# Kernel tuning notes

Hardware: AMD Instinct MI355X
Metric: run time of the kernel (lower is better)

The kernel has to match this reference:

```python
import jax, jax.numpy as jnp
import numpy as np

B, T_SEQ, STATE, DIM_IN, DIM_K, DIM_V, LAYER = 8, 2048, 128, 1024, 64, 64, 4
T = T_SEQ + 2 * STATE  # 2304
LAMBDA_INIT = 0.8 - 0.6 * float(np.exp(-0.3 * LAYER))
NEG = -1e30


def setup_inputs() -> dict:
    key = jax.random.key(0)
    ks = jax.random.split(key, 20)
    def w(k, shape):
        return jax.random.normal(k, shape, dtype=jnp.float32) * 0.02
    inp = {"x": jax.random.normal(ks[0], (B, T, DIM_IN), dtype=jnp.float32)}
    # projection weights stored as (in, out) so y = x @ W
    inp["Wq"] = w(ks[1], (DIM_IN, 2 * DIM_K)); inp["Wk"] = w(ks[2], (DIM_IN, 2 * DIM_K)); inp["Wv"] = w(ks[3], (DIM_IN, 2 * DIM_V))
    inp["Wq_ss"] = w(ks[4], (DIM_IN, 2 * DIM_K)); inp["Wk_ss"] = w(ks[5], (DIM_IN, 2 * DIM_K)); inp["Wv_ss"] = w(ks[6], (DIM_IN, 2 * DIM_V))
    inp["Wq_se"] = w(ks[7], (DIM_IN, 2 * DIM_K)); inp["Wk_se"] = w(ks[8], (DIM_IN, 2 * DIM_K)); inp["Wv_se"] = w(ks[9], (DIM_IN, 2 * DIM_V))
    # layernorm params (torch defaults: ones/zeros)
    inp["g_in"] = jnp.ones((DIM_IN,), jnp.float32); inp["b_in"] = jnp.zeros((DIM_IN,), jnp.float32)
    inp["g_ss"] = jnp.ones((DIM_IN,), jnp.float32); inp["b_ss"] = jnp.zeros((DIM_IN,), jnp.float32)
    inp["g_se"] = jnp.ones((DIM_IN,), jnp.float32); inp["b_se"] = jnp.zeros((DIM_IN,), jnp.float32)
    inp["g_out"] = jnp.ones((2 * DIM_V,), jnp.float32); inp["b_out"] = jnp.zeros((2 * DIM_V,), jnp.float32)
    # lambda gate params
    inp["lq1"] = jax.random.normal(ks[10], (1, DIM_K), jnp.float32)
    inp["lq2"] = jax.random.normal(ks[11], (1, DIM_K), jnp.float32)
    inp["lk1"] = jax.random.normal(ks[12], (DIM_K, 1), jnp.float32)
    inp["lk2"] = jax.random.normal(ks[13], (DIM_K, 1), jnp.float32)
    return inp


def _ln(z, g, b, eps=1e-5):
    m = jnp.mean(z, axis=-1, keepdims=True)
    v = jnp.mean((z - m) ** 2, axis=-1, keepdims=True)
    return (z - m) * jax.lax.rsqrt(v + eps) * g + b


def reference(x, Wq, Wk, Wv, Wq_ss, Wk_ss, Wv_ss, Wq_se, Wk_se, Wv_se,
              g_in, b_in, g_ss, b_ss, g_se, b_se, g_out, b_out,
              lq1, lq2, lk1, lk2):
    # extract_state: split off state tokens at both ends
    xs, xm, xe = x[:, :STATE], x[:, STATE:-STATE], x[:, -STATE:]
    xm = _ln(xm, g_in, b_in)
    xs = _ln(xs, g_ss, b_ss)
    xe = _ln(xe, g_se, b_se)
    q = jnp.concatenate([xs @ Wq_ss, xm @ Wq, xe @ Wq_se], axis=1)  # (B,T,2K)
    k = jnp.concatenate([xs @ Wk_ss, xm @ Wk, xe @ Wk_se], axis=1)
    v = jnp.concatenate([xs @ Wv_ss, xm @ Wv, xe @ Wv_se], axis=1)  # (B,T,2V)
    q1, q2 = q[..., :DIM_K], q[..., DIM_K:]
    k1, k2 = k[..., :DIM_K], k[..., DIM_K:]
    scale = 1.0 / np.sqrt(DIM_K)
    t = q.shape[1]
    causal = jnp.triu(jnp.full((t, t), NEG, dtype=q.dtype), k=1)  # (T,T)
    s1 = jnp.einsum('btd,bsd->bts', q1, k1) * scale + causal
    s2 = jnp.einsum('btd,bsd->bts', q2, k2) * scale + causal
    a1 = jax.nn.softmax(s1, axis=-1)
    a2 = jax.nn.softmax(s2, axis=-1)
    o1 = jnp.einsum('bts,bsd->btd', a1, v)
    o2 = jnp.einsum('bts,bsd->btd', a2, v)
    lam = (jnp.exp(lq1 @ lk1) - jnp.exp(lq2 @ lk2))[0, 0] + LAMBDA_INIT
    att = o1 - lam * o2
    return _ln(att, g_out, b_out)
```

## Files before the change

### kernel.cpp

```cpp
#include <hip/hip_runtime.h>
#include <hip/hip_bf16.h>
#include <stdint.h>

#define B_ 8
#define T_ 2304
#define DIN 1024
#define LAMBDA_INIT_F 0.6192834728526788f

typedef __bf16 bf16x8 __attribute__((ext_vector_type(8)));
typedef float f32x4 __attribute__((ext_vector_type(4)));

__device__ __forceinline__ unsigned short f2bf(float f) {
    union { float f; unsigned int u; } v; v.f = f;
    unsigned int u = v.u;
    unsigned int r = (u + 0x7FFFu + ((u >> 16) & 1u)) >> 16;
    return (unsigned short)r;
}

__device__ __forceinline__ unsigned int pack2bf(float lo, float hi) {
    return ((unsigned int)f2bf(hi) << 16) | (unsigned int)f2bf(lo);
}

__device__ __forceinline__ float bf2f(unsigned short u) {
    union { unsigned int u; float f; } v; v.u = ((unsigned int)u) << 16;
    return v.f;
}

__global__ __launch_bounds__(256) void k_wtrans(
    const float* w0, const float* w1, const float* w2,
    const float* w3, const float* w4, const float* w5,
    const float* w6, const float* w7, const float* w8,
    unsigned short* __restrict__ wt)
{
    __shared__ float tile[64][65];
    int bx = blockIdx.x;
    int mat = bx >> 5;
    int tl = bx & 31;
    int tx = tl & 15;
    int ty = tl >> 4;
    const float* srcs[9] = {w0, w1, w2, w3, w4, w5, w6, w7, w8};
    const float* src = srcs[mat];
    int k0 = tx * 64, c0 = ty * 64;
    int t = threadIdx.x;
    int r = t >> 2, cg = (t & 3) << 4;
    const float* p = src + (size_t)(k0 + r) * 128 + c0 + cg;
#pragma unroll
    for (int i = 0; i < 4; ++i) {
        float4 v = *(const float4*)(p + i * 4);
        tile[r][cg + i * 4 + 0] = v.x;
        tile[r][cg + i * 4 + 1] = v.y;
        tile[r][cg + i * 4 + 2] = v.z;
        tile[r][cg + i * 4 + 3] = v.w;
    }
    __syncthreads();
    int seg = mat / 3, m = mat % 3;
    int crow = seg * 384 + m * 128 + c0 + r;
    unsigned short* dst = wt + (size_t)crow * 1024 + k0 + cg;
    __align__(16) unsigned short ob[16];
#pragma unroll
    for (int i = 0; i < 16; ++i) ob[i] = f2bf(tile[cg + i][r]);
    *(uint4*)(dst) = *(const uint4*)(ob);
    *(uint4*)(dst + 8) = *(const uint4*)(ob + 8);
}

__global__ __launch_bounds__(256) void k_ln(
    const float* __restrict__ x,
    const float* __restrict__ g_in, const float* __restrict__ b_in,
    const float* __restrict__ g_ss, const float* __restrict__ b_ss,
    const float* __restrict__ g_se, const float* __restrict__ b_se,
    unsigned short* __restrict__ xbf)
{
    int row = (blockIdx.x << 2) + (threadIdx.x >> 6);
    int l = threadIdx.x & 63;
    int t = row % T_;
    const float* gv; const float* bv;
    if (t < 128)       { gv = g_ss; bv = b_ss; }
    else if (t < 2176) { gv = g_in; bv = b_in; }
    else               { gv = g_se; bv = b_se; }
    const float* xp = x + (size_t)row * DIN + l * 4;
    float4 v0 = *(const float4*)(xp);
    float4 v1 = *(const float4*)(xp + 256);
    float4 v2 = *(const float4*)(xp + 512);
    float4 v3 = *(const float4*)(xp + 768);
    float s  = v0.x + v0.y + v0.z + v0.w + v1.x + v1.y + v1.z + v1.w
             + v2.x + v2.y + v2.z + v2.w + v3.x + v3.y + v3.z + v3.w;
    float s2 = v0.x*v0.x + v0.y*v0.y + v0.z*v0.z + v0.w*v0.w
             + v1.x*v1.x + v1.y*v1.y + v1.z*v1.z + v1.w*v1.w
             + v2.x*v2.x + v2.y*v2.y + v2.z*v2.z + v2.w*v2.w
             + v3.x*v3.x + v3.y*v3.y + v3.z*v3.z + v3.w*v3.w;
#pragma unroll
    for (int off = 1; off <= 32; off <<= 1) {
        s  += __shfl_xor(s,  off);
        s2 += __shfl_xor(s2, off);
    }
    float mean = s * (1.f / 1024.f);
    float rstd = rsqrtf(s2 * (1.f / 1024.f) - mean * mean + 1e-5f);
    unsigned short* op = xbf + (size_t)row * DIN + l * 4;
    const float* gp = gv + l * 4;
    const float* bp = bv + l * 4;
#pragma unroll
    for (int k = 0; k < 4; ++k) {
        float4 vv = (k == 0) ? v0 : (k == 1) ? v1 : (k == 2) ? v2 : v3;
        float4 gk = *(const float4*)(gp + k * 256);
        float4 bk = *(const float4*)(bp + k * 256);
        uint2 o;
        o.x = pack2bf((vv.x - mean) * rstd * gk.x + bk.x,
                      (vv.y - mean) * rstd * gk.y + bk.y);
        o.y = pack2bf((vv.z - mean) * rstd * gk.z + bk.z,
                      (vv.w - mean) * rstd * gk.w + bk.w);
        *(uint2*)(op + k * 256) = o;
    }
}

__global__ __launch_bounds__(512, 4) void k_proj2(
    const unsigned short* __restrict__ xbf,
    const unsigned short* __restrict__ wt,
    unsigned short* __restrict__ qo,
    unsigned short* __restrict__ ko,
    unsigned short* __restrict__ vto)
{
    __shared__ __align__(16) char smem[81920];

    int bid = blockIdx.x;
    int mt = bid >> 1, ch = bid & 1;
    int bb = mt / 18, tt = mt % 18;
    int seg = (tt == 0) ? 0 : ((tt < 17) ? 1 : 2);
    size_t arow0 = (size_t)mt * 128;
    int ncol0 = ch * 192;
    int wrow0 = seg * 384 + ncol0;

    int tid = threadIdx.x;
    int w = tid >> 6, l = tid & 63;
    int wr = w >> 2, wc = w & 3;
    int g4 = l >> 4, cr = l & 15;

    int rA0 = tid >> 3, cS = (tid & 7) << 4;
    const char* srcA0 = (const char*)xbf + (arow0 + rA0) * 2048 + cS;
    const char* srcA1 = srcA0 + (size_t)64 * 2048;
    int dA0 = rA0 * 128 + (cS ^ ((rA0 & 7) << 4));
    int dA1 = dA0 + 64 * 128;
    const char* srcW0 = (const char*)wt + (size_t)(wrow0 + rA0) * 2048 + cS;
    const char* srcW1 = srcW0 + (size_t)64 * 2048;
    const char* srcW2 = srcW0 + (size_t)128 * 2048;
    int dW0 = dA0, dW1 = dA0 + 64 * 128, dW2 = dA0 + 128 * 128;

    {
        uint4 a0 = *(const uint4*)srcA0;
        uint4 a1 = *(const uint4*)srcA1;
        uint4 w0 = *(const uint4*)srcW0;
        uint4 w1 = *(const uint4*)srcW1;
        uint4 w2 = *(const uint4*)srcW2;
        *(uint4*)(smem + dA0) = a0;
        *(uint4*)(smem + dA1) = a1;
        *(uint4*)(smem + 32768 + dW0) = w0;
        *(uint4*)(smem + 32768 + dW1) = w1;
        *(uint4*)(smem + 32768 + dW2) = w2;
    }
    __syncthreads();

    f32x4 acc[4][3] = {};
    for (int ks = 0; ks < 16; ++ks) {
        bool pf = (ks < 15);
        uint4 pa0, pa1, pw0, pw1, pw2;
        if (pf) {
            size_t o = (size_t)(ks + 1) * 128;
            pa0 = *(const uint4*)(srcA0 + o);
            pa1 = *(const uint4*)(srcA1 + o);
            pw0 = *(const uint4*)(srcW0 + o);
            pw1 = *(const uint4*)(srcW1 + o);
            pw2 = *(const uint4*)(srcW2 + o);
        }
        const char* Ab = smem + (ks & 1) * 16384;
        const char* Wb = smem + 32768 + (ks & 1) * 24576;
        __builtin_amdgcn_s_setprio(1);
#pragma unroll
        for (int kk = 0; kk < 2; ++kk) {
            int kb = kk * 64 + g4 * 16;
            bf16x8 af[4];
#pragma unroll
            for (int r4 = 0; r4 < 4; ++r4) {
                int rr = wr * 64 + r4 * 16 + cr;
                af[r4] = *(const bf16x8*)(Ab + rr * 128 + (kb ^ ((rr & 7) << 4)));
            }
            bf16x8 bfr[3];
#pragma unroll
            for (int nt = 0; nt < 3; ++nt) {
                int c = wc * 48 + nt * 16 + cr;
                bfr[nt] = *(const bf16x8*)(Wb + c * 128 + (kb ^ ((c & 7) << 4)));
            }
#pragma unroll
            for (int r4 = 0; r4 < 4; ++r4)
#pragma unroll
                for (int nt = 0; nt < 3; ++nt)
                    acc[r4][nt] = __builtin_amdgcn_mfma_f32_16x16x32_bf16(af[r4], bfr[nt], acc[r4][nt], 0, 0, 0);
        }
        __builtin_amdgcn_s_setprio(0);
        __syncthreads();
        if (pf) {
            char* An = smem + ((ks + 1) & 1) * 16384;
            char* Wn = smem + 32768 + ((ks + 1) & 1) * 24576;
            *(uint4*)(An + dA0) = pa0;
            *(uint4*)(An + dA1) = pa1;
            *(uint4*)(Wn + dW0) = pw0;
            *(uint4*)(Wn + dW1) = pw1;
            *(uint4*)(Wn + dW2) = pw2;
        }
        __syncthreads();
    }

#pragma unroll
    for (int r4 = 0; r4 < 4; ++r4) {
        size_t grow = arow0 + wr * 64 + r4 * 16 + g4 * 4;
#pragma unroll
        for (int nt = 0; nt < 3; ++nt) {
            int c = ncol0 + wc * 48 + nt * 16 + cr;
            f32x4 a = acc[r4][nt];
            if (c < 128) {
#pragma unroll
                for (int g = 0; g < 4; ++g)
                    qo[(grow + g) * 128 + c] = f2bf(a[g]);
            } else if (c < 256) {
#pragma unroll
                for (int g = 0; g < 4; ++g)
                    ko[(grow + g) * 128 + (c - 128)] = f2bf(a[g]);
            } else {
                int cv = c - 256;
                int trow = tt * 128 + wr * 64 + r4 * 16 + g4 * 4;
                uint2 o;
                o.x = pack2bf(a[0], a[1]);
                o.y = pack2bf(a[2], a[3]);
                *(uint2*)(vto + ((size_t)bb * 128 + cv) * T_ + trow) = o;
            }
        }
    }
}

__global__ __launch_bounds__(512, 2) void k_attn(
    const unsigned short* __restrict__ qp_,
    const unsigned short* __restrict__ kp_,
    const unsigned short* __restrict__ vp_,
    const float* __restrict__ lq1, const float* __restrict__ lq2,
    const float* __restrict__ lk1, const float* __restrict__ lk2,
    const float* __restrict__ g_out, const float* __restrict__ b_out,
    unsigned short* __restrict__ opart,
    float* __restrict__ mlpart,
    float* __restrict__ out)
{
    __shared__ __align__(16) char smem[69632];

    int bid = blockIdx.x;
    int b = bid & 7;
    int u = 71 - (bid >> 3);
    int j, ci;
    if (u < 12)      { j = u; ci = 0; }
    else if (u < 36) { int v = u - 12; j = 12 + (v >> 1); ci = v & 1; }
    else             { int v = u - 36; j = 24 + v / 3; ci = v % 3; }
    int nch = (j + 12) / 12;
    int c0 = ci * 12;
    int ntile = min(12, j + 1 - c0);
    int t0 = j * 64;

    int tid = threadIdx.x;
    int w8 = tid >> 6;
    int qg = w8 & 3;
    int p  = w8 >> 2;
    int l = tid & 63;
    int g4 = l >> 4, q = l & 15;
    int q_g = t0 + qg * 16 + q;
    int grp = tid >> 8;
    int uu = tid & 255;

    int rK = uu >> 2, cK = (uu & 3) << 6;
    const char* srcK0 = (const char*)(kp_ + ((size_t)b * T_ + rK) * 128) + cK;
    int rV = uu >> 1, cV = (uu & 1) << 6;
    const char* srcV0 = (const char*)(vp_ + ((size_t)b * 128 + rV) * T_) + cV;
    int swK = (rK & 7) << 4;
    char* KwB = smem + grp * 16384 + rK * 256;
    int oko0 = (cK +  0) ^ swK, oko1 = (cK + 16) ^ swK;
    int oko2 = (cK + 32) ^ swK, oko3 = (cK + 48) ^ swK;
    int swV = (rV & 7) << 4;
    char* VwB = smem + 32768 + grp * 16384 + rV * 128;
    int ovo0 = (cV +  0) ^ swV, ovo1 = (cV + 16) ^ swV;
    int ovo2 = (cV + 32) ^ swV, ovo3 = (cV + 48) ^ swV;

    bf16x8 qf[2][2];
#pragma unroll
    for (int br = 0; br < 2; ++br)
#pragma unroll
        for (int h = 0; h < 2; ++h)
            qf[br][h] = *(const bf16x8*)(qp_ + ((size_t)b * T_ + q_g) * 128 + br * 64 + h * 32 + g4 * 8);

    if (grp < ntile) {
        const char* sK = srcK0 + (size_t)(c0 + grp) * 16384;
        uint4 ka0 = *(const uint4*)(sK);
        uint4 ka1 = *(const uint4*)(sK + 16);
        uint4 ka2 = *(const uint4*)(sK + 32);
        uint4 ka3 = *(const uint4*)(sK + 48);
        const char* sV = srcV0 + (size_t)(c0 + grp) * 128;
        uint4 va0 = *(const uint4*)(sV);
        uint4 va1 = *(const uint4*)(sV + 16);
        uint4 va2 = *(const uint4*)(sV + 32);
        uint4 va3 = *(const uint4*)(sV + 48);
        *(uint4*)(KwB + oko0) = ka0;
        *(uint4*)(KwB + oko1) = ka1;
        *(uint4*)(KwB + oko2) = ka2;
        *(uint4*)(KwB + oko3) = ka3;
        *(uint4*)(VwB + ovo0) = va0;
        *(uint4*)(VwB + ovo1) = va1;
        *(uint4*)(VwB + ovo2) = va2;
        *(uint4*)(VwB + ovo3) = va3;
    }
    __syncthreads();

    float mrun[2] = {-1e30f, -1e30f};
    float lrun[2] = {0.f, 0.f};
    f32x4 oacc[2][8] = {};
    const char* Kb = smem + p * 16384;
    const char* Vb = smem + 32768 + p * 16384;

    int nph = (ntile + 1) >> 1;
    for (int t = 0; t < nph; ++t) {
        int lpf = 2 * (t + 1) + grp;
        bool pfv = (lpf < ntile);
        uint4 ka0, ka1, ka2, ka3, va0, va1, va2, va3;
        if (pfv) {
            const char* sK = srcK0 + (size_t)(c0 + lpf) * 16384;
            ka0 = *(const uint4*)(sK);
            ka1 = *(const uint4*)(sK + 16);
            ka2 = *(const uint4*)(sK + 32);
            ka3 = *(const uint4*)(sK + 48);
            const char* sV = srcV0 + (size_t)(c0 + lpf) * 128;
            va0 = *(const uint4*)(sV);
            va1 = *(const uint4*)(sV + 16);
            va2 = *(const uint4*)(sV + 32);
            va3 = *(const uint4*)(sV + 48);
        }

        int lt = 2 * t + p;
        if (lt < ntile) {
            int kt = c0 + lt;
            bool diag = (kt == j);
            unsigned int pk[2][4][2];
#pragma unroll
            for (int br = 0; br < 2; ++br) {
                f32x4 s[4] = {};
                __builtin_amdgcn_s_setprio(1);
#pragma unroll
                for (int h = 0; h < 2; ++h) {
#pragma unroll
                    for (int t4 = 0; t4 < 4; ++t4) {
                        int rk = t4 * 16 + q;
                        bf16x8 kf = *(const bf16x8*)(Kb + rk * 256 + ((br * 128 + h * 64 + g4 * 16) ^ ((rk & 7) << 4)));
                        s[t4] = __builtin_amdgcn_mfma_f32_16x16x32_bf16(kf, qf[br][h], s[t4], 0, 0, 0);
                    }
                }
                __builtin_amdgcn_s_setprio(0);
                float sv[16];
                float mx = -1e30f;
#pragma unroll
                for (int t4 = 0; t4 < 4; ++t4)
#pragma unroll
                    for (int r = 0; r < 4; ++r) {
                        float v = s[t4][r] * 0.125f;
                        if (diag) {
                            int kv_g = kt * 64 + t4 * 16 + g4 * 4 + r;
                            if (kv_g > q_g) v = -1e30f;
                        }
                        sv[t4 * 4 + r] = v;
                        mx = fmaxf(mx, v);
                    }
                mx = fmaxf(mx, __shfl_xor(mx, 16));
                mx = fmaxf(mx, __shfl_xor(mx, 32));
                float mn;
                if (__all(mx <= mrun[br] + 8.f)) {
                    mn = mrun[br];
                } else {
                    mn = fmaxf(mrun[br], mx);
                    float sf = __expf(mrun[br] - mn);
                    mrun[br] = mn;
                    lrun[br] *= sf;
#pragma unroll
                    for (int dblk = 0; dblk < 8; ++dblk)
#pragma unroll
                        for (int r = 0; r < 4; ++r)
                            oacc[br][dblk][r] *= sf;
                }
                float pr[16];
                float rs = 0.f;
#pragma unroll
                for (int i = 0; i < 16; ++i) {
                    pr[i] = __expf(sv[i] - mn);
                    rs += pr[i];
                }
                rs += __shfl_xor(rs, 16);
                rs += __shfl_xor(rs, 32);
                lrun[br] += rs;
#pragma unroll
                for (int t4 = 0; t4 < 4; ++t4) {
                    pk[br][t4][0] = pack2bf(pr[t4 * 4 + 0], pr[t4 * 4 + 1]);
                    pk[br][t4][1] = pack2bf(pr[t4 * 4 + 2], pr[t4 * 4 + 3]);
                }
            }
#pragma unroll
            for (int h = 0; h < 2; ++h) {
                bf16x8 pb[2];
                int s0 = q + (((g4 * 2) & 3) << 4);
                int s1 = q + (((g4 * 2 + 1) & 3) << 4);
                int sel = g4 >> 1;
#pragma unroll
                for (int br = 0; br < 2; ++br) {
                    unsigned int m0a = (unsigned int)__shfl((int)pk[br][2 * h][0], s0);
                    unsigned int m0b = (unsigned int)__shfl((int)pk[br][2 * h + 1][0], s0);
                    unsigned int m1a = (unsigned int)__shfl((int)pk[br][2 * h][1], s0);
                    unsigned int m1b = (unsigned int)__shfl((int)pk[br][2 * h + 1][1], s0);
                    unsigned int m2a = (unsigned int)__shfl((int)pk[br][2 * h][0], s1);
                    unsigned int m2b = (unsigned int)__shfl((int)pk[br][2 * h + 1][0], s1);
                    unsigned int m3a = (unsigned int)__shfl((int)pk[br][2 * h][1], s1);
                    unsigned int m3b = (unsigned int)__shfl((int)pk[br][2 * h + 1][1], s1);
                    union { unsigned int uv[4]; bf16x8 v; } pu;
                    pu.uv[0] = sel ? m0b : m0a;
                    pu.uv[1] = sel ? m1b : m1a;
                    pu.uv[2] = sel ? m2b : m2a;
                    pu.uv[3] = sel ? m3b : m3a;
                    pb[br] = pu.v;
                }
                __builtin_amdgcn_s_setprio(1);
#pragma unroll
                for (int dblk = 0; dblk < 8; ++dblk) {
                    int rv = dblk * 16 + q;
                    bf16x8 vf = *(const bf16x8*)(Vb + rv * 128 + ((h * 64 + g4 * 16) ^ ((rv & 7) << 4)));
                    oacc[0][dblk] = __builtin_amdgcn_mfma_f32_16x16x32_bf16(vf, pb[0], oacc[0][dblk], 0, 0, 0);
                    oacc[1][dblk] = __builtin_amdgcn_mfma_f32_16x16x32_bf16(vf, pb[1], oacc[1][dblk], 0, 0, 0);
                }
                __builtin_amdgcn_s_setprio(0);
            }
        }
        __syncthreads();
        if (pfv) {
            *(uint4*)(KwB + oko0) = ka0;
            *(uint4*)(KwB + oko1) = ka1;
            *(uint4*)(KwB + oko2) = ka2;
            *(uint4*)(KwB + oko3) = ka3;
            *(uint4*)(VwB + ovo0) = va0;
            *(uint4*)(VwB + ovo1) = va1;
            *(uint4*)(VwB + ovo2) = va2;
            *(uint4*)(VwB + ovo3) = va3;
        }
        __syncthreads();
    }

    float* Osh = (float*)smem;
    float* Msh = (float*)(smem + 65536);
    if (p == 1) {
        int base = qg * 4096 + l;
#pragma unroll
        for (int br = 0; br < 2; ++br)
#pragma unroll
            for (int dblk = 0; dblk < 8; ++dblk)
#pragma unroll
                for (int r = 0; r < 4; ++r)
                    Osh[base + (br * 32 + dblk * 4 + r) * 64] = oacc[br][dblk][r];
        float4 ml;
        ml.x = mrun[0]; ml.y = lrun[0]; ml.z = mrun[1]; ml.w = lrun[1];
        *(float4*)(Msh + (qg * 64 + l) * 4) = ml;
    }
    __syncthreads();
    if (p == 0) {
        float4 ml = *(const float4*)(Msh + (qg * 64 + l) * 4);
        float m1v[2] = {ml.x, ml.z}, l1v[2] = {ml.y, ml.w};
        float lfin[2], mst[2];
#pragma unroll
        for (int br = 0; br < 2; ++br) {
            float mstar = fmaxf(mrun[br], m1v[br]);
            float a0 = __expf(mrun[br] - mstar);
            float a1 = __expf(m1v[br] - mstar);
            lfin[br] = a0 * lrun[br] + a1 * l1v[br];
            mst[br] = mstar;
            int base = qg * 4096 + l;
#pragma unroll
            for (int dblk = 0; dblk < 8; ++dblk)
#pragma unroll
                for (int r = 0; r < 4; ++r)
                    oacc[br][dblk][r] = a0 * oacc[br][dblk][r]
                        + a1 * Osh[base + (br * 32 + dblk * 4 + r) * 64];
        }

        int row = qg * 16 + q;
        if (nch == 1) {
            float pa = lq1[l] * lk1[l];
            float pb2 = lq2[l] * lk2[l];
#pragma unroll
            for (int off = 32; off >= 1; off >>= 1) {
                pa += __shfl_xor(pa, off);
                pb2 += __shfl_xor(pb2, off);
            }
            float lam = __expf(pa) - __expf(pb2) + LAMBDA_INIT_F;

            float att[8][4];
            float sm = 0.f;
            float inv1 = 1.f / lfin[0], inv2 = 1.f / lfin[1];
#pragma unroll
            for (int dblk = 0; dblk < 8; ++dblk)
#pragma unroll
                for (int r = 0; r < 4; ++r) {
                    float a = oacc[0][dblk][r] * inv1 - lam * (oacc[1][dblk][r] * inv2);
                    att[dblk][r] = a;
                    sm += a;
                }
            sm += __shfl_xor(sm, 16);
            sm += __shfl_xor(sm, 32);
            float mean = sm * (1.f / 128.f);
            float sv2 = 0.f;
#pragma unroll
            for (int dblk = 0; dblk < 8; ++dblk)
#pragma unroll
                for (int r = 0; r < 4; ++r) {
                    float d = att[dblk][r] - mean;
                    sv2 += d * d;
                }
            sv2 += __shfl_xor(sv2, 16);
            sv2 += __shfl_xor(sv2, 32);
            float rstd = rsqrtf(sv2 * (1.f / 128.f) + 1e-5f);

            float* orow = out + ((size_t)b * T_ + q_g) * 128;
#pragma unroll
            for (int dblk = 0; dblk < 8; ++dblk) {
                int d0 = dblk * 16 + g4 * 4;
                float4 o;
                o.x = (att[dblk][0] - mean) * rstd * g_out[d0 + 0] + b_out[d0 + 0];
                o.y = (att[dblk][1] - mean) * rstd * g_out[d0 + 1] + b_out[d0 + 1];
                o.z = (att[dblk][2] - mean) * rstd * g_out[d0 + 2] + b_out[d0 + 2];
                o.w = (att[dblk][3] - mean) * rstd * g_out[d0 + 3] + b_out[d0 + 3];
                *(float4*)(orow + d0) = o;
            }
        } else {
            int slot = (b * 36 + j) * 3 + ci;
            char* ob = (char*)opart + (size_t)slot * 32768;
#pragma unroll
            for (int br = 0; br < 2; ++br) {
#pragma unroll
                for (int dblk = 0; dblk < 8; ++dblk) {
                    uint2 o;
                    o.x = pack2bf(oacc[br][dblk][0], oacc[br][dblk][1]);
                    o.y = pack2bf(oacc[br][dblk][2], oacc[br][dblk][3]);
                    *(uint2*)(ob + br * 16384 + row * 256 + (dblk * 16 + g4 * 4) * 2) = o;
                }
                float2 mlv;
                mlv.x = mst[br];
                mlv.y = lfin[br];
                *(float2*)(mlpart + ((size_t)slot * 128 + br * 64 + row) * 2) = mlv;
            }
        }
    }
}

__global__ __launch_bounds__(512) void k_merge(
    const unsigned short* __restrict__ opart,
    const float* __restrict__ mlpart,
    const float* __restrict__ lq1, const float* __restrict__ lq2,
    const float* __restrict__ lk1, const float* __restrict__ lk2,
    const float* __restrict__ g_out, const float* __restrict__ b_out,
    float* __restrict__ out)
{
    int bid = blockIdx.x;
    int b = bid & 7;
    int j = 12 + (bid >> 3);
    int nch = (j + 12) / 12;
    int tid = threadIdx.x;
    int row = tid >> 3;
    int d0 = (tid & 7) * 16;
    int l = tid & 63;

    float pa = lq1[l] * lk1[l];
    float pb = lq2[l] * lk2[l];
#pragma unroll
    for (int off = 32; off >= 1; off >>= 1) {
        pa += __shfl_xor(pa, off);
        pb += __shfl_xor(pb, off);
    }
    float lam = __expf(pa) - __expf(pb) + LAMBDA_INIT_F;

    int slotb = (b * 36 + j) * 3;
    float res[2][16];
#pragma unroll
    for (int br = 0; br < 2; ++br) {
        float m0 = mlpart[((size_t)(slotb + 0) * 128 + br * 64 + row) * 2];
        float l0 = mlpart[((size_t)(slotb + 0) * 128 + br * 64 + row) * 2 + 1];
        float m1 = mlpart[((size_t)(slotb + 1) * 128 + br * 64 + row) * 2];
        float l1 = mlpart[((size_t)(slotb + 1) * 128 + br * 64 + row) * 2 + 1];
        float m2 = -1e30f, l2 = 0.f;
        if (nch == 3) {
            m2 = mlpart[((size_t)(slotb + 2) * 128 + br * 64 + row) * 2];
            l2 = mlpart[((size_t)(slotb + 2) * 128 + br * 64 + row) * 2 + 1];
        }
        float mstar = fmaxf(fmaxf(m0, m1), m2);
        float w0 = __expf(m0 - mstar);
        float w1 = __expf(m1 - mstar);
        float w2 = (nch == 3) ? __expf(m2 - mstar) : 0.f;
        float lsum = w0 * l0 + w1 * l1 + w2 * l2;

        float acc[16] = {};
#pragma unroll
        for (int c = 0; c < 3; ++c) {
            if (c >= nch) break;
            float wc = (c == 0) ? w0 : (c == 1) ? w1 : w2;
            const char* ob = (const char*)opart + (size_t)(slotb + c) * 32768
                           + br * 16384 + row * 256 + d0 * 2;
            uint4 v0 = *(const uint4*)(ob);
            uint4 v1 = *(const uint4*)(ob + 16);
            const unsigned int vv[8] = {v0.x, v0.y, v0.z, v0.w, v1.x, v1.y, v1.z, v1.w};
#pragma unroll
            for (int i = 0; i < 8; ++i) {
                acc[i * 2]     += wc * bf2f((unsigned short)(vv[i] & 0xFFFF));
                acc[i * 2 + 1] += wc * bf2f((unsigned short)(vv[i] >> 16));
            }
        }
        float inv = 1.f / lsum;
#pragma unroll
        for (int i = 0; i < 16; ++i) res[br][i] = acc[i] * inv;
    }

    float att[16];
    float sm = 0.f;
#pragma unroll
    for (int i = 0; i < 16; ++i) {
        att[i] = res[0][i] - lam * res[1][i];
        sm += att[i];
    }
    sm += __shfl_xor(sm, 1);
    sm += __shfl_xor(sm, 2);
    sm += __shfl_xor(sm, 4);
    float mean = sm * (1.f / 128.f);
    float sv2 = 0.f;
#pragma unroll
    for (int i = 0; i < 16; ++i) {
        float d = att[i] - mean;
        sv2 += d * d;
    }
    sv2 += __shfl_xor(sv2, 1);
    sv2 += __shfl_xor(sv2, 2);
    sv2 += __shfl_xor(sv2, 4);
    float rstd = rsqrtf(sv2 * (1.f / 128.f) + 1e-5f);

    float* orow = out + ((size_t)b * T_ + j * 64 + row) * 128 + d0;
#pragma unroll
    for (int k = 0; k < 4; ++k) {
        float4 o;
        o.x = (att[k * 4 + 0] - mean) * rstd * g_out[d0 + k * 4 + 0] + b_out[d0 + k * 4 + 0];
        o.y = (att[k * 4 + 1] - mean) * rstd * g_out[d0 + k * 4 + 1] + b_out[d0 + k * 4 + 1];
        o.z = (att[k * 4 + 2] - mean) * rstd * g_out[d0 + k * 4 + 2] + b_out[d0 + k * 4 + 2];
        o.w = (att[k * 4 + 3] - mean) * rstd * g_out[d0 + k * 4 + 3] + b_out[d0 + k * 4 + 3];
        *(float4*)(orow + k * 4) = o;
    }
}

extern "C" void kernel_launch(void* const* d_in, const int* in_sizes, int n_in,
                              void* d_out, int out_size, void* d_ws, size_t ws_size,
                              hipStream_t stream) {
    (void)in_sizes; (void)n_in; (void)out_size; (void)ws_size;
    const float* x = (const float*)d_in[0];
    char* ws = (char*)d_ws;
    unsigned short* wt  = (unsigned short*)ws;
    unsigned short* xbf = (unsigned short*)(ws + 2359296);
    unsigned short* qo  = (unsigned short*)(ws + 40108032);
    unsigned short* ko  = (unsigned short*)(ws + 44826624);
    unsigned short* vto = (unsigned short*)(ws + 49545216);
    unsigned short* opart = (unsigned short*)(ws + 2359296);
    float*          mlpart = (float*)(ws + 2359296 + 28311552);

    hipLaunchKernelGGL(k_wtrans, dim3(288), dim3(256), 0, stream,
        (const float*)d_in[4], (const float*)d_in[5], (const float*)d_in[6],
        (const float*)d_in[1], (const float*)d_in[2], (const float*)d_in[3],
        (const float*)d_in[7], (const float*)d_in[8], (const float*)d_in[9], wt);

    hipLaunchKernelGGL(k_ln, dim3(4608), dim3(256), 0, stream,
        x,
        (const float*)d_in[10], (const float*)d_in[11],
        (const float*)d_in[12], (const float*)d_in[13],
        (const float*)d_in[14], (const float*)d_in[15],
        xbf);

    hipLaunchKernelGGL(k_proj2, dim3(288), dim3(512), 0, stream,
        xbf, wt, qo, ko, vto);

    hipLaunchKernelGGL(k_attn, dim3(576), dim3(512), 0, stream,
        qo, ko, vto,
        (const float*)d_in[18], (const float*)d_in[19],
        (const float*)d_in[20], (const float*)d_in[21],
        (const float*)d_in[16], (const float*)d_in[17],
        opart, mlpart,
        (float*)d_out);

    hipLaunchKernelGGL(k_merge, dim3(192), dim3(512), 0, stream,
        opart, mlpart,
        (const float*)d_in[18], (const float*)d_in[19],
        (const float*)d_in[20], (const float*)d_in[21],
        (const float*)d_in[16], (const float*)d_in[17],
        (float*)d_out);
}
```

Before: 128.1 us.

## Split attention KV into 6-tile chunks with single-group 256-thread blocks

Restructures the attention kernel from 512-thread blocks, where two wave groups split the KV tiles and merge through shared memory, to 256-thread blocks that walk up to 6 KV tiles sequentially. Split-KV chunking moves from 12 to 6 tiles, which raises the block count to 1008 and gives up to 6 partial chunks per query tile. The merge kernel and workspace slot indexing are generalized to match. The goal is better load balance and occupancy with less shared memory and no intra-block merge, at the cost of more partial-result traffic and more merge work.

```diff
diff --git a/kernel.cpp b/kernel.cpp
--- a/kernel.cpp
+++ b/kernel.cpp
@@ -235,7 +235,7 @@
     }
 }
 
-__global__ __launch_bounds__(512, 2) void k_attn(
+__global__ __launch_bounds__(256, 4) void k_attn(
     const unsigned short* __restrict__ qp_,
     const unsigned short* __restrict__ kp_,
     const unsigned short* __restrict__ vp_,
@@ -246,40 +246,48 @@
     float* __restrict__ mlpart,
     float* __restrict__ out)
 {
-    __shared__ __align__(16) char smem[69632];
+    __shared__ __align__(16) char smem[32768];
 
     int bid = blockIdx.x;
     int b = bid & 7;
-    int u = 71 - (bid >> 3);
+    int u = 125 - (bid >> 3);
     int j, ci;
-    if (u < 12)      { j = u; ci = 0; }
-    else if (u < 36) { int v = u - 12; j = 12 + (v >> 1); ci = v & 1; }
-    else             { int v = u - 36; j = 24 + v / 3; ci = v % 3; }
-    int nch = (j + 12) / 12;
-    int c0 = ci * 12;
-    int ntile = min(12, j + 1 - c0);
+    if (u < 6) { j = u; ci = 0; }
+    else {
+        int v = u - 6;
+        int g, base;
+        if (v < 12)      { g = 0; base = 0;  }
+        else if (v < 30) { g = 1; base = 12; }
+        else if (v < 54) { g = 2; base = 30; }
+        else if (v < 84) { g = 3; base = 54; }
+        else             { g = 4; base = 84; }
+        int w2 = v - base;
+        int per = g + 2;
+        int qd = w2 / per;
+        j = 6 * (g + 1) + qd;
+        ci = w2 - qd * per;
+    }
+    int nch = (j + 6) / 6;
+    int c0 = ci * 6;
+    int ntile = min(6, j + 1 - c0);
     int t0 = j * 64;
 
     int tid = threadIdx.x;
-    int w8 = tid >> 6;
-    int qg = w8 & 3;
-    int p  = w8 >> 2;
+    int qg = tid >> 6;
     int l = tid & 63;
     int g4 = l >> 4, q = l & 15;
     int q_g = t0 + qg * 16 + q;
-    int grp = tid >> 8;
-    int uu = tid & 255;
-
-    int rK = uu >> 2, cK = (uu & 3) << 6;
+
+    int rK = tid >> 2, cK = (tid & 3) << 6;
     const char* srcK0 = (const char*)(kp_ + ((size_t)b * T_ + rK) * 128) + cK;
-    int rV = uu >> 1, cV = (uu & 1) << 6;
+    int rV = tid >> 1, cV = (tid & 1) << 6;
     const char* srcV0 = (const char*)(vp_ + ((size_t)b * 128 + rV) * T_) + cV;
     int swK = (rK & 7) << 4;
-    char* KwB = smem + grp * 16384 + rK * 256;
+    char* KwB = smem + rK * 256;
     int oko0 = (cK +  0) ^ swK, oko1 = (cK + 16) ^ swK;
     int oko2 = (cK + 32) ^ swK, oko3 = (cK + 48) ^ swK;
     int swV = (rV & 7) << 4;
-    char* VwB = smem + 32768 + grp * 16384 + rV * 128;
+    char* VwB = smem + 16384 + rV * 128;
     int ovo0 = (cV +  0) ^ swV, ovo1 = (cV + 16) ^ swV;
     int ovo2 = (cV + 32) ^ swV, ovo3 = (cV + 48) ^ swV;
 
@@ -290,13 +298,13 @@
         for (int h = 0; h < 2; ++h)
             qf[br][h] = *(const bf16x8*)(qp_ + ((size_t)b * T_ + q_g) * 128 + br * 64 + h * 32 + g4 * 8);
 
-    if (grp < ntile) {
-        const char* sK = srcK0 + (size_t)(c0 + grp) * 16384;
+    {
+        const char* sK = srcK0 + (size_t)c0 * 16384;
         uint4 ka0 = *(const uint4*)(sK);
         uint4 ka1 = *(const uint4*)(sK + 16);
         uint4 ka2 = *(const uint4*)(sK + 32);
         uint4 ka3 = *(const uint4*)(sK + 48);
-        const char* sV = srcV0 + (size_t)(c0 + grp) * 128;
+        const char* sV = srcV0 + (size_t)c0 * 128;
         uint4 va0 = *(const uint4*)(sV);
         uint4 va1 = *(const uint4*)(sV + 16);
         uint4 va2 = *(const uint4*)(sV + 32);
@@ -315,125 +323,120 @@
     float mrun[2] = {-1e30f, -1e30f};
     float lrun[2] = {0.f, 0.f};
     f32x4 oacc[2][8] = {};
-    const char* Kb = smem + p * 16384;
-    const char* Vb = smem + 32768 + p * 16384;
-
-    int nph = (ntile + 1) >> 1;
-    for (int t = 0; t < nph; ++t) {
-        int lpf = 2 * (t + 1) + grp;
-        bool pfv = (lpf < ntile);
+    const char* Kb = smem;
+    const char* Vb = smem + 16384;
+
+    for (int t = 0; t < ntile; ++t) {
+        bool pfv = (t + 1 < ntile);
         uint4 ka0, ka1, ka2, ka3, va0, va1, va2, va3;
         if (pfv) {
-            const char* sK = srcK0 + (size_t)(c0 + lpf) * 16384;
+            const char* sK = srcK0 + (size_t)(c0 + t + 1) * 16384;
             ka0 = *(const uint4*)(sK);
             ka1 = *(const uint4*)(sK + 16);
             ka2 = *(const uint4*)(sK + 32);
             ka3 = *(const uint4*)(sK + 48);
-            const char* sV = srcV0 + (size_t)(c0 + lpf) * 128;
+            const char* sV = srcV0 + (size_t)(c0 + t + 1) * 128;
             va0 = *(const uint4*)(sV);
             va1 = *(const uint4*)(sV + 16);
             va2 = *(const uint4*)(sV + 32);
             va3 = *(const uint4*)(sV + 48);
         }
 
-        int lt = 2 * t + p;
-        if (lt < ntile) {
-            int kt = c0 + lt;
-            bool diag = (kt == j);
-            unsigned int pk[2][4][2];
+        int kt = c0 + t;
+        bool diag = (kt == j);
+        unsigned int pk[2][4][2];
+#pragma unroll
+        for (int br = 0; br < 2; ++br) {
+            f32x4 s[4] = {};
+            __builtin_amdgcn_s_setprio(1);
+#pragma unroll
+            for (int h = 0; h < 2; ++h) {
+#pragma unroll
+                for (int t4 = 0; t4 < 4; ++t4) {
+                    int rk = t4 * 16 + q;
+                    bf16x8 kf = *(const bf16x8*)(Kb + rk * 256 + ((br * 128 + h * 64 + g4 * 16) ^ ((rk & 7) << 4)));
+                    s[t4] = __builtin_amdgcn_mfma_f32_16x16x32_bf16(kf, qf[br][h], s[t4], 0, 0, 0);
+                }
+            }
+            __builtin_amdgcn_s_setprio(0);
+            float sv[16];
+            float mx = -1e30f;
+#pragma unroll
+            for (int t4 = 0; t4 < 4; ++t4)
+#pragma unroll
+                for (int r = 0; r < 4; ++r) {
+                    float v = s[t4][r] * 0.125f;
+                    if (diag) {
+                        int kv_g = kt * 64 + t4 * 16 + g4 * 4 + r;
+                        if (kv_g > q_g) v = -1e30f;
+                    }
+                    sv[t4 * 4 + r] = v;
+                    mx = fmaxf(mx, v);
+                }
+            mx = fmaxf(mx, __shfl_xor(mx, 16));
+            mx = fmaxf(mx, __shfl_xor(mx, 32));
+            float mn;
+            if (__all(mx <= mrun[br] + 8.f)) {
+                mn = mrun[br];
+            } else {
+                mn = fmaxf(mrun[br], mx);
+                float sf = __expf(mrun[br] - mn);
+                mrun[br] = mn;
+                lrun[br] *= sf;
+#pragma unroll
+                for (int dblk = 0; dblk < 8; ++dblk)
+#pragma unroll
+                    for (int r = 0; r < 4; ++r)
+                        oacc[br][dblk][r] *= sf;
+            }
+            float pr[16];
+            float rs = 0.f;
+#pragma unroll
+            for (int i = 0; i < 16; ++i) {
+                pr[i] = __expf(sv[i] - mn);
+                rs += pr[i];
+            }
+            rs += __shfl_xor(rs, 16);
+            rs += __shfl_xor(rs, 32);
+            lrun[br] += rs;
+#pragma unroll
+            for (int t4 = 0; t4 < 4; ++t4) {
+                pk[br][t4][0] = pack2bf(pr[t4 * 4 + 0], pr[t4 * 4 + 1]);
+                pk[br][t4][1] = pack2bf(pr[t4 * 4 + 2], pr[t4 * 4 + 3]);
+            }
+        }
+#pragma unroll
+        for (int h = 0; h < 2; ++h) {
+            bf16x8 pb[2];
+            int s0 = q + (((g4 * 2) & 3) << 4);
+            int s1 = q + (((g4 * 2 + 1) & 3) << 4);
+            int sel = g4 >> 1;
 #pragma unroll
             for (int br = 0; br < 2; ++br) {
-                f32x4 s[4] = {};
-                __builtin_amdgcn_s_setprio(1);
-#pragma unroll
-                for (int h = 0; h < 2; ++h) {
-#pragma unroll
-                    for (int t4 = 0; t4 < 4; ++t4) {
-                        int rk = t4 * 16 + q;
-                        bf16x8 kf = *(const bf16x8*)(Kb + rk * 256 + ((br * 128 + h * 64 + g4 * 16) ^ ((rk & 7) << 4)));
-                        s[t4] = __builtin_amdgcn_mfma_f32_16x16x32_bf16(kf, qf[br][h], s[t4], 0, 0, 0);
-                    }
-                }
-                __builtin_amdgcn_s_setprio(0);
-                float sv[16];
-                float mx = -1e30f;
-#pragma unroll
-                for (int t4 = 0; t4 < 4; ++t4)
-#pragma unroll
-                    for (int r = 0; r < 4; ++r) {
-                        float v = s[t4][r] * 0.125f;
-                        if (diag) {
-                            int kv_g = kt * 64 + t4 * 16 + g4 * 4 + r;
-                            if (kv_g > q_g) v = -1e30f;
-                        }
-                        sv[t4 * 4 + r] = v;
-                        mx = fmaxf(mx, v);
-                    }
-                mx = fmaxf(mx, __shfl_xor(mx, 16));
-                mx = fmaxf(mx, __shfl_xor(mx, 32));
-                float mn;
-                if (__all(mx <= mrun[br] + 8.f)) {
-                    mn = mrun[br];
-                } else {
-                    mn = fmaxf(mrun[br], mx);
-                    float sf = __expf(mrun[br] - mn);
-                    mrun[br] = mn;
-                    lrun[br] *= sf;
-#pragma unroll
-                    for (int dblk = 0; dblk < 8; ++dblk)
-#pragma unroll
-                        for (int r = 0; r < 4; ++r)
-                            oacc[br][dblk][r] *= sf;
-                }
-                float pr[16];
-                float rs = 0.f;
-#pragma unroll
-                for (int i = 0; i < 16; ++i) {
-                    pr[i] = __expf(sv[i] - mn);
-                    rs += pr[i];
-                }
-                rs += __shfl_xor(rs, 16);
-                rs += __shfl_xor(rs, 32);
-                lrun[br] += rs;
-#pragma unroll
-                for (int t4 = 0; t4 < 4; ++t4) {
-                    pk[br][t4][0] = pack2bf(pr[t4 * 4 + 0], pr[t4 * 4 + 1]);
-                    pk[br][t4][1] = pack2bf(pr[t4 * 4 + 2], pr[t4 * 4 + 3]);
-                }
-            }
-#pragma unroll
-            for (int h = 0; h < 2; ++h) {
-                bf16x8 pb[2];
-                int s0 = q + (((g4 * 2) & 3) << 4);
-                int s1 = q + (((g4 * 2 + 1) & 3) << 4);
-                int sel = g4 >> 1;
-#pragma unroll
-                for (int br = 0; br < 2; ++br) {
-                    unsigned int m0a = (unsigned int)__shfl((int)pk[br][2 * h][0], s0);
-                    unsigned int m0b = (unsigned int)__shfl((int)pk[br][2 * h + 1][0], s0);
-                    unsigned int m1a = (unsigned int)__shfl((int)pk[br][2 * h][1], s0);
-                    unsigned int m1b = (unsigned int)__shfl((int)pk[br][2 * h + 1][1], s0);
-                    unsigned int m2a = (unsigned int)__shfl((int)pk[br][2 * h][0], s1);
-                    unsigned int m2b = (unsigned int)__shfl((int)pk[br][2 * h + 1][0], s1);
-                    unsigned int m3a = (unsigned int)__shfl((int)pk[br][2 * h][1], s1);
-                    unsigned int m3b = (unsigned int)__shfl((int)pk[br][2 * h + 1][1], s1);
-                    union { unsigned int uv[4]; bf16x8 v; } pu;
-                    pu.uv[0] = sel ? m0b : m0a;
-                    pu.uv[1] = sel ? m1b : m1a;
-                    pu.uv[2] = sel ? m2b : m2a;
-                    pu.uv[3] = sel ? m3b : m3a;
-                    pb[br] = pu.v;
-                }
-                __builtin_amdgcn_s_setprio(1);
-#pragma unroll
-                for (int dblk = 0; dblk < 8; ++dblk) {
-                    int rv = dblk * 16 + q;
-                    bf16x8 vf = *(const bf16x8*)(Vb + rv * 128 + ((h * 64 + g4 * 16) ^ ((rv & 7) << 4)));
-                    oacc[0][dblk] = __builtin_amdgcn_mfma_f32_16x16x32_bf16(vf, pb[0], oacc[0][dblk], 0, 0, 0);
-                    oacc[1][dblk] = __builtin_amdgcn_mfma_f32_16x16x32_bf16(vf, pb[1], oacc[1][dblk], 0, 0, 0);
-                }
-                __builtin_amdgcn_s_setprio(0);
-            }
+                unsigned int m0a = (unsigned int)__shfl((int)pk[br][2 * h][0], s0);
+                unsigned int m0b = (unsigned int)__shfl((int)pk[br][2 * h + 1][0], s0);
+                unsigned int m1a = (unsigned int)__shfl((int)pk[br][2 * h][1], s0);
+                unsigned int m1b = (unsigned int)__shfl((int)pk[br][2 * h + 1][1], s0);
+                unsigned int m2a = (unsigned int)__shfl((int)pk[br][2 * h][0], s1);
+                unsigned int m2b = (unsigned int)__shfl((int)pk[br][2 * h + 1][0], s1);
+                unsigned int m3a = (unsigned int)__shfl((int)pk[br][2 * h][1], s1);
+                unsigned int m3b = (unsigned int)__shfl((int)pk[br][2 * h + 1][1], s1);
+                union { unsigned int uv[4]; bf16x8 v; } pu;
+                pu.uv[0] = sel ? m0b : m0a;
+                pu.uv[1] = sel ? m1b : m1a;
+                pu.uv[2] = sel ? m2b : m2a;
+                pu.uv[3] = sel ? m3b : m3a;
+                pb[br] = pu.v;
+            }
+            __builtin_amdgcn_s_setprio(1);
+#pragma unroll
+            for (int dblk = 0; dblk < 8; ++dblk) {
+                int rv = dblk * 16 + q;
+                bf16x8 vf = *(const bf16x8*)(Vb + rv * 128 + ((h * 64 + g4 * 16) ^ ((rv & 7) << 4)));
+                oacc[0][dblk] = __builtin_amdgcn_mfma_f32_16x16x32_bf16(vf, pb[0], oacc[0][dblk], 0, 0, 0);
+                oacc[1][dblk] = __builtin_amdgcn_mfma_f32_16x16x32_bf16(vf, pb[1], oacc[1][dblk], 0, 0, 0);
+            }
+            __builtin_amdgcn_s_setprio(0);
         }
         __syncthreads();
         if (pfv) {
@@ -449,105 +452,72 @@
         __syncthreads();
     }
 
-    float* Osh = (float*)smem;
-    float* Msh = (float*)(smem + 65536);
-    if (p == 1) {
-        int base = qg * 4096 + l;
-#pragma unroll
-        for (int br = 0; br < 2; ++br)
-#pragma unroll
-            for (int dblk = 0; dblk < 8; ++dblk)
-#pragma unroll
-                for (int r = 0; r < 4; ++r)
-                    Osh[base + (br * 32 + dblk * 4 + r) * 64] = oacc[br][dblk][r];
-        float4 ml;
-        ml.x = mrun[0]; ml.y = lrun[0]; ml.z = mrun[1]; ml.w = lrun[1];
-        *(float4*)(Msh + (qg * 64 + l) * 4) = ml;
-    }
-    __syncthreads();
-    if (p == 0) {
-        float4 ml = *(const float4*)(Msh + (qg * 64 + l) * 4);
-        float m1v[2] = {ml.x, ml.z}, l1v[2] = {ml.y, ml.w};
-        float lfin[2], mst[2];
+    int row = qg * 16 + q;
+    if (nch == 1) {
+        float pa = lq1[l] * lk1[l];
+        float pb2 = lq2[l] * lk2[l];
+#pragma unroll
+        for (int off = 32; off >= 1; off >>= 1) {
+            pa += __shfl_xor(pa, off);
+            pb2 += __shfl_xor(pb2, off);
+        }
+        float lam = __expf(pa) - __expf(pb2) + LAMBDA_INIT_F;
+
+        float att[8][4];
+        float sm = 0.f;
+        float inv1 = 1.f / lrun[0], inv2 = 1.f / lrun[1];
+#pragma unroll
+        for (int dblk = 0; dblk < 8; ++dblk)
+#pragma unroll
+            for (int r = 0; r < 4; ++r) {
+                float a = oacc[0][dblk][r] * inv1 - lam * (oacc[1][dblk][r] * inv2);
+                att[dblk][r] = a;
+                sm += a;
+            }
+        sm += __shfl_xor(sm, 16);
+        sm += __shfl_xor(sm, 32);
+        float mean = sm * (1.f / 128.f);
+        float sv2 = 0.f;
+#pragma unroll
+        for (int dblk = 0; dblk < 8; ++dblk)
+#pragma unroll
+            for (int r = 0; r < 4; ++r) {
+                float d = att[dblk][r] - mean;
+                sv2 += d * d;
+            }
+        sv2 += __shfl_xor(sv2, 16);
+        sv2 += __shfl_xor(sv2, 32);
+        float rstd = rsqrtf(sv2 * (1.f / 128.f) + 1e-5f);
+
+        float* orow = out + ((size_t)b * T_ + q_g) * 128;
+#pragma unroll
+        for (int dblk = 0; dblk < 8; ++dblk) {
+            int d0 = dblk * 16 + g4 * 4;
+            float4 o;
+            o.x = (att[dblk][0] - mean) * rstd * g_out[d0 + 0] + b_out[d0 + 0];
+            o.y = (att[dblk][1] - mean) * rstd * g_out[d0 + 1] + b_out[d0 + 1];
+            o.z = (att[dblk][2] - mean) * rstd * g_out[d0 + 2] + b_out[d0 + 2];
+            o.w = (att[dblk][3] - mean) * rstd * g_out[d0 + 3] + b_out[d0 + 3];
+            *(float4*)(orow + d0) = o;
+        }
+    } else {
+        int g2 = (j - 6) / 6;
+        int off = 6 * g2 * (g2 + 3) / 2 + (j - 6 - 6 * g2) * (g2 + 2);
+        int slot = b * 120 + off + ci;
+        char* ob = (char*)opart + (size_t)slot * 32768;
 #pragma unroll
         for (int br = 0; br < 2; ++br) {
-            float mstar = fmaxf(mrun[br], m1v[br]);
-            float a0 = __expf(mrun[br] - mstar);
-            float a1 = __expf(m1v[br] - mstar);
-            lfin[br] = a0 * lrun[br] + a1 * l1v[br];
-            mst[br] = mstar;
-            int base = qg * 4096 + l;
-#pragma unroll
-            for (int dblk = 0; dblk < 8; ++dblk)
-#pragma unroll
-                for (int r = 0; r < 4; ++r)
-                    oacc[br][dblk][r] = a0 * oacc[br][dblk][r]
-                        + a1 * Osh[base + (br * 32 + dblk * 4 + r) * 64];
-        }
-
-        int row = qg * 16 + q;
-        if (nch == 1) {
-            float pa = lq1[l] * lk1[l];
-            float pb2 = lq2[l] * lk2[l];
-#pragma unroll
-            for (int off = 32; off >= 1; off >>= 1) {
-                pa += __shfl_xor(pa, off);
-                pb2 += __shfl_xor(pb2, off);
-            }
-            float lam = __expf(pa) - __expf(pb2) + LAMBDA_INIT_F;
-
-            float att[8][4];
-            float sm = 0.f;
-            float inv1 = 1.f / lfin[0], inv2 = 1.f / lfin[1];
-#pragma unroll
-            for (int dblk = 0; dblk < 8; ++dblk)
-#pragma unroll
-                for (int r = 0; r < 4; ++r) {
-                    float a = oacc[0][dblk][r] * inv1 - lam * (oacc[1][dblk][r] * inv2);
-                    att[dblk][r] = a;
-                    sm += a;
-                }
-            sm += __shfl_xor(sm, 16);
-            sm += __shfl_xor(sm, 32);
-            float mean = sm * (1.f / 128.f);
-            float sv2 = 0.f;
-#pragma unroll
-            for (int dblk = 0; dblk < 8; ++dblk)
-#pragma unroll
-                for (int r = 0; r < 4; ++r) {
-                    float d = att[dblk][r] - mean;
-                    sv2 += d * d;
-                }
-            sv2 += __shfl_xor(sv2, 16);
-            sv2 += __shfl_xor(sv2, 32);
-            float rstd = rsqrtf(sv2 * (1.f / 128.f) + 1e-5f);
-
-            float* orow = out + ((size_t)b * T_ + q_g) * 128;
 #pragma unroll
             for (int dblk = 0; dblk < 8; ++dblk) {
-                int d0 = dblk * 16 + g4 * 4;
-                float4 o;
-                o.x = (att[dblk][0] - mean) * rstd * g_out[d0 + 0] + b_out[d0 + 0];
-                o.y = (att[dblk][1] - mean) * rstd * g_out[d0 + 1] + b_out[d0 + 1];
-                o.z = (att[dblk][2] - mean) * rstd * g_out[d0 + 2] + b_out[d0 + 2];
-                o.w = (att[dblk][3] - mean) * rstd * g_out[d0 + 3] + b_out[d0 + 3];
-                *(float4*)(orow + d0) = o;
-            }
-        } else {
-            int slot = (b * 36 + j) * 3 + ci;
-            char* ob = (char*)opart + (size_t)slot * 32768;
-#pragma unroll
-            for (int br = 0; br < 2; ++br) {
-#pragma unroll
-                for (int dblk = 0; dblk < 8; ++dblk) {
-                    uint2 o;
-                    o.x = pack2bf(oacc[br][dblk][0], oacc[br][dblk][1]);
-                    o.y = pack2bf(oacc[br][dblk][2], oacc[br][dblk][3]);
-                    *(uint2*)(ob + br * 16384 + row * 256 + (dblk * 16 + g4 * 4) * 2) = o;
-                }
+                uint2 o;
+                o.x = pack2bf(oacc[br][dblk][0], oacc[br][dblk][1]);
+                o.y = pack2bf(oacc[br][dblk][2], oacc[br][dblk][3]);
+                *(uint2*)(ob + br * 16384 + row * 256 + (dblk * 16 + g4 * 4) * 2) = o;
+            }
+            if (g4 == 0) {
                 float2 mlv;
-                mlv.x = mst[br];
-                mlv.y = lfin[br];
+                mlv.x = mrun[br];
+                mlv.y = lrun[br];
                 *(float2*)(mlpart + ((size_t)slot * 128 + br * 64 + row) * 2) = mlv;
             }
         }
@@ -564,8 +534,10 @@
 {
     int bid = blockIdx.x;
     int b = bid & 7;
-    int j = 12 + (bid >> 3);
-    int nch = (j + 12) / 12;
+    int j = 6 + (bid >> 3);
+    int nch = (j + 6) / 6;
+    int g2 = (j - 6) / 6;
+    int slotb = b * 120 + 6 * g2 * (g2 + 3) / 2 + (j - 6 - 6 * g2) * (g2 + 2);
     int tid = threadIdx.x;
     int row = tid >> 3;
     int d0 = (tid & 7) * 16;
@@ -580,30 +552,37 @@
     }
     float lam = __expf(pa) - __expf(pb) + LAMBDA_INIT_F;
 
-    int slotb = (b * 36 + j) * 3;
     float res[2][16];
 #pragma unroll
     for (int br = 0; br < 2; ++br) {
-        float m0 = mlpart[((size_t)(slotb + 0) * 128 + br * 64 + row) * 2];
-        float l0 = mlpart[((size_t)(slotb + 0) * 128 + br * 64 + row) * 2 + 1];
-        float m1 = mlpart[((size_t)(slotb + 1) * 128 + br * 64 + row) * 2];
-        float l1 = mlpart[((size_t)(slotb + 1) * 128 + br * 64 + row) * 2 + 1];
-        float m2 = -1e30f, l2 = 0.f;
-        if (nch == 3) {
-            m2 = mlpart[((size_t)(slotb + 2) * 128 + br * 64 + row) * 2];
-            l2 = mlpart[((size_t)(slotb + 2) * 128 + br * 64 + row) * 2 + 1];
-        }
-        float mstar = fmaxf(fmaxf(m0, m1), m2);
-        float w0 = __expf(m0 - mstar);
-        float w1 = __expf(m1 - mstar);
-        float w2 = (nch == 3) ? __expf(m2 - mstar) : 0.f;
-        float lsum = w0 * l0 + w1 * l1 + w2 * l2;
+        float mv0 = -1e30f, mv1 = -1e30f, mv2 = -1e30f,
+              mv3 = -1e30f, mv4 = -1e30f, mv5 = -1e30f;
+        float lv0 = 0.f, lv1 = 0.f, lv2 = 0.f, lv3 = 0.f, lv4 = 0.f, lv5 = 0.f;
+        {
+            const float* p0 = mlpart + ((size_t)slotb * 128 + br * 64 + row) * 2;
+            mv0 = p0[0]; lv0 = p0[1];
+            const float* p1 = mlpart + ((size_t)(slotb + 1) * 128 + br * 64 + row) * 2;
+            mv1 = p1[0]; lv1 = p1[1];
+            if (nch > 2) { const float* p = mlpart + ((size_t)(slotb + 2) * 128 + br * 64 + row) * 2; mv2 = p[0]; lv2 = p[1]; }
+            if (nch > 3) { const float* p = mlpart + ((size_t)(slotb + 3) * 128 + br * 64 + row) * 2; mv3 = p[0]; lv3 = p[1]; }
+            if (nch > 4) { const float* p = mlpart + ((size_t)(slotb + 4) * 128 + br * 64 + row) * 2; mv4 = p[0]; lv4 = p[1]; }
+            if (nch > 5) { const float* p = mlpart + ((size_t)(slotb + 5) * 128 + br * 64 + row) * 2; mv5 = p[0]; lv5 = p[1]; }
+        }
+        float mstar = fmaxf(fmaxf(fmaxf(mv0, mv1), fmaxf(mv2, mv3)), fmaxf(mv4, mv5));
+        float w0 = __expf(mv0 - mstar);
+        float w1 = __expf(mv1 - mstar);
+        float w2 = (nch > 2) ? __expf(mv2 - mstar) : 0.f;
+        float w3 = (nch > 3) ? __expf(mv3 - mstar) : 0.f;
+        float w4 = (nch > 4) ? __expf(mv4 - mstar) : 0.f;
+        float w5 = (nch > 5) ? __expf(mv5 - mstar) : 0.f;
+        float lsum = w0 * lv0 + w1 * lv1 + w2 * lv2 + w3 * lv3 + w4 * lv4 + w5 * lv5;
 
         float acc[16] = {};
 #pragma unroll
-        for (int c = 0; c < 3; ++c) {
+        for (int c = 0; c < 6; ++c) {
             if (c >= nch) break;
-            float wc = (c == 0) ? w0 : (c == 1) ? w1 : w2;
+            float wc = (c == 0) ? w0 : (c == 1) ? w1 : (c == 2) ? w2
+                     : (c == 3) ? w3 : (c == 4) ? w4 : w5;
             const char* ob = (const char*)opart + (size_t)(slotb + c) * 32768
                            + br * 16384 + row * 256 + d0 * 2;
             uint4 v0 = *(const uint4*)(ob);
@@ -666,7 +645,7 @@
     unsigned short* ko  = (unsigned short*)(ws + 44826624);
     unsigned short* vto = (unsigned short*)(ws + 49545216);
     unsigned short* opart = (unsigned short*)(ws + 2359296);
-    float*          mlpart = (float*)(ws + 2359296 + 28311552);
+    float*          mlpart = (float*)(ws + 2359296 + 31457280);
 
     hipLaunchKernelGGL(k_wtrans, dim3(288), dim3(256), 0, stream,
         (const float*)d_in[4], (const float*)d_in[5], (const float*)d_in[6],
@@ -683,7 +662,7 @@
     hipLaunchKernelGGL(k_proj2, dim3(288), dim3(512), 0, stream,
         xbf, wt, qo, ko, vto);
 
-    hipLaunchKernelGGL(k_attn, dim3(576), dim3(512), 0, stream,
+    hipLaunchKernelGGL(k_attn, dim3(1008), dim3(256), 0, stream,
         qo, ko, vto,
         (const float*)d_in[18], (const float*)d_in[19],
         (const float*)d_in[20], (const float*)d_in[21],
@@ -691,7 +670,7 @@
         opart, mlpart,
         (float*)d_out);
 
-    hipLaunchKernelGGL(k_merge, dim3(192), dim3(512), 0, stream,
+    hipLaunchKernelGGL(k_merge, dim3(240), dim3(512), 0, stream,
         opart, mlpart,
         (const float*)d_in[18], (const float*)d_in[19],
         (const float*)d_in[20], (const float*)d_in[21],
```

After: 162.4 us. 26.8% more time.
